# Kernel tuning notes

Hardware: AMD Instinct MI355X
Metric: run time of the kernel (lower is better)

The kernel has to match this reference:

```python
import jax, jax.numpy as jnp
import numpy as np

HEADS = 8
DIM_HEAD = 64
SCALE = DIM_HEAD ** -0.5


def setup_inputs() -> dict:
    key = jax.random.key(0)
    ks = jax.random.split(key, 7)
    b, n, m = 2, 4096, 4096
    query_dim, context_dim, inner = 1024, 768, HEADS * DIM_HEAD
    s = 0.02
    return {
        "x": jax.random.normal(ks[0], (b, n, query_dim), jnp.float32),
        "context": jax.random.normal(ks[1], (b, m, context_dim), jnp.float32),
        "Wq": jax.random.normal(ks[2], (query_dim, inner), jnp.float32) * s,
        "Wk": jax.random.normal(ks[3], (context_dim, inner), jnp.float32) * s,
        "Wv": jax.random.normal(ks[4], (context_dim, inner), jnp.float32) * s,
        "Wo": jax.random.normal(ks[5], (inner, query_dim), jnp.float32) * s,
        "bo": jnp.zeros((query_dim,), jnp.float32),
    }


def reference(x, context, Wq, Wk, Wv, Wo, bo):
    b, n, _ = x.shape
    m = context.shape[1]
    # projections (no bias), split heads: b n (h d) -> b n h d
    q = (x @ Wq).reshape(b, n, HEADS, DIM_HEAD)
    k = (context @ Wk).reshape(b, m, HEADS, DIM_HEAD)
    v = (context @ Wv).reshape(b, m, HEADS, DIM_HEAD)
    # fp32 QK^T (ATTN_PRECISION='fp32' path), full [b,h,n,m] scores
    sim = jnp.einsum("bihd,bjhd->bhij", q.astype(jnp.float32), k.astype(jnp.float32)) * SCALE
    attn = jax.nn.softmax(sim, axis=-1).astype(v.dtype)
    out = jnp.einsum("bhij,bjhd->bihd", attn, v).reshape(b, n, HEADS * DIM_HEAD)
    # to_out: Linear with bias (dropout=0 is identity)
    return out @ Wo + bo
```

## Files before the change

### kernel.cpp

```cpp
#include <hip/hip_runtime.h>
#include <hip/hip_bf16.h>
#include <cmath>


using bf16_t = __hip_bfloat16;
typedef __bf16 bf16x8 __attribute__((ext_vector_type(8)));
typedef float  f32x4  __attribute__((ext_vector_type(4)));

static constexpr int BATCH = 2;
static constexpr int NQ    = 4096;
static constexpr int NKV   = 4096;
static constexpr int NH    = 8;
static constexpr int DH    = 64;
static constexpr int INNER = NH * DH;
static constexpr int QDIM  = 1024;
static constexpr int CDIM  = 768;
static constexpr float QSCALE = 0.125f * 1.4426950408889634f;

#define MFMA_BF16(a, b, c) __builtin_amdgcn_mfma_f32_16x16x32_bf16((a), (b), (c), 0, 0, 0)

__device__ __forceinline__ float fast_exp2(float x) {
  return __builtin_amdgcn_exp2f(x);
}

__global__ __launch_bounds__(256) void cast2_kernel(const float* __restrict__ x,
                                                    bf16_t* __restrict__ xb, int xn8,
                                                    const float* __restrict__ c,
                                                    bf16_t* __restrict__ cb, int cn8) {
  int id = blockIdx.x * 256 + threadIdx.x;
  const float* in;
  bf16_t* out;
  if (id < xn8) {
    in = x; out = xb;
  } else {
    id -= xn8;
    if (id >= cn8) return;
    in = c; out = cb;
  }
  float4 a = ((const float4*)in)[2 * id];
  float4 b = ((const float4*)in)[2 * id + 1];
  bf16_t t[8] = {__float2bfloat16(a.x), __float2bfloat16(a.y), __float2bfloat16(a.z),
                 __float2bfloat16(a.w), __float2bfloat16(b.x), __float2bfloat16(b.y),
                 __float2bfloat16(b.z), __float2bfloat16(b.w)};
  ((uint4*)out)[id] = *(const uint4*)t;
}

__global__ __launch_bounds__(256) void wtrans4_kernel(const float* __restrict__ Wq,
                                                      const float* __restrict__ Wk,
                                                      const float* __restrict__ Wv,
                                                      const float* __restrict__ Wo,
                                                      bf16_t* __restrict__ WqT,
                                                      bf16_t* __restrict__ WkvT,
                                                      bf16_t* __restrict__ WoT) {
  __shared__ float tile[32][33];
  const float* W;
  bf16_t* WT;
  int K, N;
  switch (blockIdx.z) {
    case 0: W = Wq; WT = WqT; K = QDIM; N = INNER; break;
    case 1: W = Wk; WT = WkvT; K = CDIM; N = INNER; break;
    case 2: W = Wv; WT = WkvT + (size_t)INNER * CDIM; K = CDIM; N = INNER; break;
    default: W = Wo; WT = WoT; K = INNER; N = QDIM; break;
  }
  const int bn = blockIdx.x * 32, bk = blockIdx.y * 32;
  if (bn >= N || bk >= K) return;
  const int tx = threadIdx.x & 31, ty = threadIdx.x >> 5;
  for (int yy = ty; yy < 32; yy += 8)
    tile[yy][tx] = W[(size_t)(bk + yy) * N + bn + tx];
  __syncthreads();
  for (int yy = ty; yy < 32; yy += 8)
    WT[(size_t)(bn + yy) * K + bk + tx] = __float2bfloat16(tile[tx][yy]);
}

template <int OUT_MODE>
__global__ __launch_bounds__(256) void gemm_kernel(const bf16_t* __restrict__ A,
                                                   const bf16_t* __restrict__ WT,
                                                   void* __restrict__ Cp,
                                                   void* __restrict__ Cp2,
                                                   const float* __restrict__ bias,
                                                   float ascale, int M, int N, int K) {
  __shared__ __align__(16) bf16_t As[2][64][32];
  __shared__ __align__(16) bf16_t Bs[2][128][32];
  const int tid = threadIdx.x;
  const int lane = tid & 63, wave = tid >> 6;
  const int lane15 = lane & 15, quad = lane >> 4;
  const int wm = (wave >> 1) * 32, wn = (wave & 1) * 64;
  const int m0 = blockIdx.x * 64, n0 = blockIdx.y * 128;

  const f32x4 vzero = {0.f, 0.f, 0.f, 0.f};
  f32x4 acc[2][4];
  for (int i = 0; i < 2; ++i)
    for (int j = 0; j < 4; ++j) acc[i][j] = vzero;

  const int srow = tid >> 2, sc8 = (tid & 3) * 8;
  const bf16_t* aptr  = A + (size_t)(m0 + srow) * K + sc8;
  const bf16_t* bptr0 = WT + (size_t)(n0 + srow) * K + sc8;
  const bf16_t* bptr1 = WT + (size_t)(n0 + srow + 64) * K + sc8;
  uint4 ar = *(const uint4*)aptr;
  uint4 br0 = *(const uint4*)bptr0;
  uint4 br1 = *(const uint4*)bptr1;

  const int T = K / 32;
  for (int t = 0; t < T; ++t) {
    const int cur = t & 1;
    *(uint4*)&As[cur][srow][sc8]      = ar;
    *(uint4*)&Bs[cur][srow][sc8]      = br0;
    *(uint4*)&Bs[cur][srow + 64][sc8] = br1;
    __syncthreads();
    if (t + 1 < T) {
      aptr += 32; bptr0 += 32; bptr1 += 32;
      ar  = *(const uint4*)aptr;
      br0 = *(const uint4*)bptr0;
      br1 = *(const uint4*)bptr1;
    }
    bf16x8 af[2], bfr[4];
    for (int i = 0; i < 2; ++i)
      af[i] = *reinterpret_cast<const bf16x8*>(&As[cur][wm + i * 16 + lane15][quad * 8]);
    for (int j = 0; j < 4; ++j)
      bfr[j] = *reinterpret_cast<const bf16x8*>(&Bs[cur][wn + j * 16 + lane15][quad * 8]);
    for (int i = 0; i < 2; ++i)
      for (int j = 0; j < 4; ++j) acc[i][j] = MFMA_BF16(af[i], bfr[j], acc[i][j]);
  }

  for (int i = 0; i < 2; ++i) {
    int gm = m0 + wm + i * 16 + quad * 4;
    for (int j = 0; j < 4; ++j) {
      int gn = n0 + wn + j * 16 + lane15;
      for (int r = 0; r < 4; ++r) {
        float v = acc[i][j][r];
        if constexpr (OUT_MODE == 0) {
          ((bf16_t*)Cp)[(size_t)(gm + r) * N + gn] = __float2bfloat16(v * ascale);
        } else if constexpr (OUT_MODE == 1) {
          ((float*)Cp)[(size_t)(gm + r) * N + gn] = v + bias[gn];
        } else {
          if (gn < INNER) {
            ((bf16_t*)Cp)[(size_t)(gm + r) * INNER + gn] = __float2bfloat16(v);
          } else {
            int gmr = gm + r;
            ((bf16_t*)Cp2)[((size_t)(gmr >> 12) * INNER + (gn - INNER)) * (size_t)NKV +
                           (gmr & 4095)] = __float2bfloat16(v);
          }
        }
      }
    }
  }
}

__global__ __launch_bounds__(512) void attn_kernel(const bf16_t* Qg ,
                                                   const bf16_t* __restrict__ Kg ,
                                                   const bf16_t* __restrict__ Vtg ,
                                                   bf16_t* Og ) {
  __shared__ __align__(16) bf16_t KsF[2][8][512];
  __shared__ __align__(16) bf16_t VtF[2][8][512];
  __shared__ __align__(16) bf16_t PsA[128][72];

  const int tid = threadIdx.x;
  const int lane = tid & 63, wave = tid >> 6;
  const int lane15 = lane & 15, quad = lane >> 4;
  const int wrow = wave * 16;
  const int q0 = blockIdx.x * 128;
  const int h = blockIdx.y;
  const int b = blockIdx.z;

  const size_t qbase  = ((size_t)b * NQ + q0) * INNER + h * DH;
  const size_t kbase  = ((size_t)b * NKV) * INNER + h * DH;
  const size_t vtbase = ((size_t)(b * NH + h) * DH) * NKV;

  bf16x8 qf[2];
  for (int ks = 0; ks < 2; ++ks)
    qf[ks] = *reinterpret_cast<const bf16x8*>(
        Qg + qbase + (size_t)(wrow + lane15) * INNER + ks * 32 + quad * 8);

  const f32x4 vzero = {0.f, 0.f, 0.f, 0.f};
  f32x4 acc_o[4];
  float l_part = 0.f;
  for (int j = 0; j < 4; ++j) acc_o[j] = vzero;

  const int cw = wave;
  auto kaddr = [&](int kv0) {
    return Kg + kbase + (size_t)(kv0 + (cw & 3) * 16 + lane15) * INNER + (cw >> 2) * 32 + quad * 8;
  };
  auto vaddr = [&](int kv0) {
    return Vtg + vtbase + (size_t)((cw & 3) * 16 + lane15) * NKV + kv0 + (cw >> 2) * 32 + quad * 8;
  };
  uint4 kr = *(const uint4*)kaddr(0);
  uint4 vr = *(const uint4*)vaddr(0);

  constexpr int T = NKV / 64;
  for (int t = 0; t < T; ++t) {
    const int cur = t & 1;
    *(uint4*)&KsF[cur][cw][lane * 8] = kr;
    *(uint4*)&VtF[cur][cw][lane * 8] = vr;
    __syncthreads();

    f32x4 acc_st[4];
    for (int j = 0; j < 4; ++j) acc_st[j] = vzero;
    for (int ks = 0; ks < 2; ++ks) {
      bf16x8 kf[4];
      for (int j = 0; j < 4; ++j)
        kf[j] = *reinterpret_cast<const bf16x8*>(&KsF[cur][ks * 4 + j][lane * 8]);
      for (int j = 0; j < 4; ++j) acc_st[j] = MFMA_BF16(kf[j], qf[ks], acc_st[j]);
    }

    if (t + 1 < T) {
      int kv0n = (t + 1) * 64;
      kr = *(const uint4*)kaddr(kv0n);
      vr = *(const uint4*)vaddr(kv0n);
    }

    for (int j = 0; j < 4; ++j) {
      bf16_t t4[4];
      for (int r = 0; r < 4; ++r) {
        float p = fast_exp2(acc_st[j][r]);
        l_part += p;
        t4[r] = __float2bfloat16(p);
      }
      *(uint2*)&PsA[wrow + lane15][j * 16 + quad * 4] = *(const uint2*)t4;
    }
    asm volatile("s_waitcnt lgkmcnt(0)" ::: "memory");

    for (int ks = 0; ks < 2; ++ks) {
      bf16x8 pf, vf[4];
      pf = *reinterpret_cast<const bf16x8*>(&PsA[wrow + lane15][ks * 32 + quad * 8]);
      for (int j = 0; j < 4; ++j)
        vf[j] = *reinterpret_cast<const bf16x8*>(&VtF[cur][ks * 4 + j][lane * 8]);
      for (int j = 0; j < 4; ++j) acc_o[j] = MFMA_BF16(pf, vf[j], acc_o[j]);
    }
  }

  float l = l_part;
  l += __shfl_xor(l, 16, 64);
  l += __shfl_xor(l, 32, 64);
  float inv = 1.f / l;
  for (int r = 0; r < 4; ++r) {
    float invr = __shfl(inv, quad * 4 + r, 16);
    int row = wrow + quad * 4 + r;
    for (int j = 0; j < 4; ++j)
      Og[qbase + (size_t)row * INNER + j * 16 + lane15] =
          __float2bfloat16(acc_o[j][r] * invr);
  }
}

extern "C" void kernel_launch(void* const* d_in, const int* in_sizes, int n_in,
                              void* d_out, int out_size, void* d_ws, size_t ws_size,
                              hipStream_t stream) {
  (void)in_sizes; (void)n_in; (void)out_size; (void)ws_size;
  const float* x   = (const float*)d_in[0];
  const float* ctx = (const float*)d_in[1];
  const float* Wq  = (const float*)d_in[2];
  const float* Wk  = (const float*)d_in[3];
  const float* Wv  = (const float*)d_in[4];
  const float* Wo  = (const float*)d_in[5];
  const float* bo  = (const float*)d_in[6];
  float* out = (float*)d_out;

  char* ws = (char*)d_ws;
  size_t off = 0;
  auto take = [&](size_t nelem) { bf16_t* p = (bf16_t*)(ws + off); off += nelem * 2; return p; };
  bf16_t* WqT  = take((size_t)INNER * QDIM);
  bf16_t* WkvT = take((size_t)(2 * INNER) * CDIM);
  bf16_t* WoT  = take((size_t)QDIM * INNER);
  bf16_t* qob  = take((size_t)BATCH * NQ * INNER);
  bf16_t* kb   = take((size_t)BATCH * NKV * INNER);
  bf16_t* vtb  = take((size_t)BATCH * INNER * NKV);

  bf16_t* xb   = (bf16_t*)d_out;
  bf16_t* ctxb = xb + (size_t)BATCH * NQ * QDIM;

  const int M = BATCH * NQ;
  const int xN8 = BATCH * NQ * QDIM / 8, cN8 = BATCH * NKV * CDIM / 8;

  cast2_kernel<<<(xN8 + cN8 + 255) / 256, 256, 0, stream>>>(x, xb, xN8, ctx, ctxb, cN8);
  wtrans4_kernel<<<dim3(32, 32, 4), 256, 0, stream>>>(Wq, Wk, Wv, Wo, WqT, WkvT, WoT);

  gemm_kernel<0><<<dim3(M / 64, INNER / 128), 256, 0, stream>>>(
      xb, WqT, qob, nullptr, nullptr, QSCALE, M, INNER, QDIM);
  gemm_kernel<3><<<dim3(M / 64, (2 * INNER) / 128), 256, 0, stream>>>(
      ctxb, WkvT, kb, vtb, nullptr, 1.f, M, 2 * INNER, CDIM);

  attn_kernel<<<dim3(NQ / 128, NH, BATCH), 512, 0, stream>>>(qob, kb, vtb, qob);

  gemm_kernel<1><<<dim3(M / 64, QDIM / 128), 256, 0, stream>>>(
      qob, WoT, out, nullptr, bo, 1.f, M, QDIM, INNER);
}
```

Measured before the change: 263.3 us.

## Use direct global-to-LDS loads and 128x128 tiles in GEMMs; MFMA row sums in attention

The projection GEMMs grow their block tile from 64x128 to 128x128, with four accumulator rows per wave, and stage A/B tiles through global_load_lds so data goes straight from global memory into shared memory without passing through registers. The attention kernel stops accumulating the softmax denominator with scalar adds and shuffles. It computes the row sums with an extra MFMA against a ones vector, which also uses the same bf16-rounded probabilities as the PV product. In exchange the GEMM grid has half as many blocks, and each thread holds more accumulator registers. The async LDS loads depend on the existing barrier placement to be ordered correctly with the reads.

```diff
diff --git a/kernel.cpp b/kernel.cpp
--- a/kernel.cpp
+++ b/kernel.cpp
@@ -21,6 +21,12 @@
 
 __device__ __forceinline__ float fast_exp2(float x) {
   return __builtin_amdgcn_exp2f(x);
+}
+
+__device__ __forceinline__ void gload16(const bf16_t* g, bf16_t* l) {
+  __builtin_amdgcn_global_load_lds((__attribute__((address_space(1))) void*)(g),
+                                   (__attribute__((address_space(3))) void*)(l),
+                                   16, 0, 0);
 }
 
 __global__ __launch_bounds__(256) void cast2_kernel(const float* __restrict__ x,
@@ -79,50 +85,53 @@
                                                    void* __restrict__ Cp2,
                                                    const float* __restrict__ bias,
                                                    float ascale, int M, int N, int K) {
-  __shared__ __align__(16) bf16_t As[2][64][32];
+  __shared__ __align__(16) bf16_t As[2][128][32];
   __shared__ __align__(16) bf16_t Bs[2][128][32];
   const int tid = threadIdx.x;
   const int lane = tid & 63, wave = tid >> 6;
   const int lane15 = lane & 15, quad = lane >> 4;
-  const int wm = (wave >> 1) * 32, wn = (wave & 1) * 64;
-  const int m0 = blockIdx.x * 64, n0 = blockIdx.y * 128;
+  const int wm = (wave >> 1) * 64, wn = (wave & 1) * 64;
+  const int m0 = blockIdx.x * 128, n0 = blockIdx.y * 128;
 
   const f32x4 vzero = {0.f, 0.f, 0.f, 0.f};
-  f32x4 acc[2][4];
-  for (int i = 0; i < 2; ++i)
+  f32x4 acc[4][4];
+  for (int i = 0; i < 4; ++i)
     for (int j = 0; j < 4; ++j) acc[i][j] = vzero;
 
   const int srow = tid >> 2, sc8 = (tid & 3) * 8;
-  const bf16_t* aptr  = A + (size_t)(m0 + srow) * K + sc8;
-  const bf16_t* bptr0 = WT + (size_t)(n0 + srow) * K + sc8;
-  const bf16_t* bptr1 = WT + (size_t)(n0 + srow + 64) * K + sc8;
-  uint4 ar = *(const uint4*)aptr;
-  uint4 br0 = *(const uint4*)bptr0;
-  uint4 br1 = *(const uint4*)bptr1;
+  const bf16_t* aptr = A + (size_t)(m0 + srow) * K + sc8;
+  const bf16_t* bptr = WT + (size_t)(n0 + srow) * K + sc8;
+  bf16_t* const abase = &As[0][wave * 16][0];
+  bf16_t* const bbase = &Bs[0][wave * 16][0];
+  const int bufstride = 128 * 32;
+
+  auto stage = [&](int t, int cur) {
+    const bf16_t* as = aptr + t * 32;
+    const bf16_t* bs = bptr + t * 32;
+    bf16_t* ab = abase + cur * bufstride;
+    bf16_t* bb = bbase + cur * bufstride;
+    gload16(as, ab);
+    gload16(as + (size_t)64 * K, ab + 64 * 32);
+    gload16(bs, bb);
+    gload16(bs + (size_t)64 * K, bb + 64 * 32);
+  };
 
   const int T = K / 32;
+  stage(0, 0);
   for (int t = 0; t < T; ++t) {
     const int cur = t & 1;
-    *(uint4*)&As[cur][srow][sc8]      = ar;
-    *(uint4*)&Bs[cur][srow][sc8]      = br0;
-    *(uint4*)&Bs[cur][srow + 64][sc8] = br1;
     __syncthreads();
-    if (t + 1 < T) {
-      aptr += 32; bptr0 += 32; bptr1 += 32;
-      ar  = *(const uint4*)aptr;
-      br0 = *(const uint4*)bptr0;
-      br1 = *(const uint4*)bptr1;
-    }
-    bf16x8 af[2], bfr[4];
-    for (int i = 0; i < 2; ++i)
+    if (t + 1 < T) stage(t + 1, cur ^ 1);
+    bf16x8 af[4], bfr[4];
+    for (int i = 0; i < 4; ++i)
       af[i] = *reinterpret_cast<const bf16x8*>(&As[cur][wm + i * 16 + lane15][quad * 8]);
     for (int j = 0; j < 4; ++j)
       bfr[j] = *reinterpret_cast<const bf16x8*>(&Bs[cur][wn + j * 16 + lane15][quad * 8]);
-    for (int i = 0; i < 2; ++i)
+    for (int i = 0; i < 4; ++i)
       for (int j = 0; j < 4; ++j) acc[i][j] = MFMA_BF16(af[i], bfr[j], acc[i][j]);
   }
 
-  for (int i = 0; i < 2; ++i) {
+  for (int i = 0; i < 4; ++i) {
     int gm = m0 + wm + i * 16 + quad * 4;
     for (int j = 0; j < 4; ++j) {
       int gn = n0 + wn + j * 16 + lane15;
@@ -171,9 +180,12 @@
     qf[ks] = *reinterpret_cast<const bf16x8*>(
         Qg + qbase + (size_t)(wrow + lane15) * INNER + ks * 32 + quad * 8);
 
+  bf16x8 ones;
+  for (int i = 0; i < 8; ++i) ones[i] = (__bf16)1.0f;
+
   const f32x4 vzero = {0.f, 0.f, 0.f, 0.f};
   f32x4 acc_o[4];
-  float l_part = 0.f;
+  f32x4 acc_l = vzero;
   for (int j = 0; j < 4; ++j) acc_o[j] = vzero;
 
   const int cw = wave;
@@ -210,11 +222,8 @@
 
     for (int j = 0; j < 4; ++j) {
       bf16_t t4[4];
-      for (int r = 0; r < 4; ++r) {
-        float p = fast_exp2(acc_st[j][r]);
-        l_part += p;
-        t4[r] = __float2bfloat16(p);
-      }
+      for (int r = 0; r < 4; ++r)
+        t4[r] = __float2bfloat16(fast_exp2(acc_st[j][r]));
       *(uint2*)&PsA[wrow + lane15][j * 16 + quad * 4] = *(const uint2*)t4;
     }
     asm volatile("s_waitcnt lgkmcnt(0)" ::: "memory");
@@ -224,16 +233,13 @@
       pf = *reinterpret_cast<const bf16x8*>(&PsA[wrow + lane15][ks * 32 + quad * 8]);
       for (int j = 0; j < 4; ++j)
         vf[j] = *reinterpret_cast<const bf16x8*>(&VtF[cur][ks * 4 + j][lane * 8]);
+      acc_l = MFMA_BF16(pf, ones, acc_l);
       for (int j = 0; j < 4; ++j) acc_o[j] = MFMA_BF16(pf, vf[j], acc_o[j]);
     }
   }
 
-  float l = l_part;
-  l += __shfl_xor(l, 16, 64);
-  l += __shfl_xor(l, 32, 64);
-  float inv = 1.f / l;
   for (int r = 0; r < 4; ++r) {
-    float invr = __shfl(inv, quad * 4 + r, 16);
+    float invr = 1.f / acc_l[r];
     int row = wrow + quad * 4 + r;
     for (int j = 0; j < 4; ++j)
       Og[qbase + (size_t)row * INNER + j * 16 + lane15] =
@@ -273,13 +279,13 @@
   cast2_kernel<<<(xN8 + cN8 + 255) / 256, 256, 0, stream>>>(x, xb, xN8, ctx, ctxb, cN8);
   wtrans4_kernel<<<dim3(32, 32, 4), 256, 0, stream>>>(Wq, Wk, Wv, Wo, WqT, WkvT, WoT);
 
-  gemm_kernel<0><<<dim3(M / 64, INNER / 128), 256, 0, stream>>>(
+  gemm_kernel<0><<<dim3(M / 128, INNER / 128), 256, 0, stream>>>(
       xb, WqT, qob, nullptr, nullptr, QSCALE, M, INNER, QDIM);
-  gemm_kernel<3><<<dim3(M / 64, (2 * INNER) / 128), 256, 0, stream>>>(
+  gemm_kernel<3><<<dim3(M / 128, (2 * INNER) / 128), 256, 0, stream>>>(
       ctxb, WkvT, kb, vtb, nullptr, 1.f, M, 2 * INNER, CDIM);
 
   attn_kernel<<<dim3(NQ / 128, NH, BATCH), 512, 0, stream>>>(qob, kb, vtb, qob);
 
-  gemm_kernel<1><<<dim3(M / 64, QDIM / 128), 256, 0, stream>>>(
+  gemm_kernel<1><<<dim3(M / 128, QDIM / 128), 256, 0, stream>>>(
       qob, WoT, out, nullptr, bo, 1.f, M, QDIM, INNER);
 }
```

New measurement: 264.8 us. About the same (+0.6%).
